# Kernel tuning notes

Hardware: AMD Instinct MI355X
Metric: run time of the kernel (lower is better)

Reference implementation:

```python
import jax, jax.numpy as jnp
import numpy as np
from jax import lax

FC = 8      # heads_count
LN_EPS = 1e-5

def _ln(x, g, b):
    mu = jnp.mean(x, axis=-1, keepdims=True)
    var = jnp.mean((x - mu) ** 2, axis=-1, keepdims=True)
    return (x - mu) / jnp.sqrt(var + LN_EPS) * g + b

def _l2norm(x):
    return x / jnp.maximum(jnp.linalg.norm(x, axis=-1, keepdims=True), 1e-12)

def _gelu(x):
    return jax.nn.gelu(x, approximate=False)

def _resize_bilinear(x, oh, ow):
    # x: [N, C, H, W], align_corners=True bilinear (matches F.interpolate)
    h, w = x.shape[2], x.shape[3]
    ys = jnp.linspace(0.0, h - 1.0, oh)
    xs = jnp.linspace(0.0, w - 1.0, ow)
    y0 = jnp.floor(ys).astype(jnp.int32); y1 = jnp.minimum(y0 + 1, h - 1)
    x0 = jnp.floor(xs).astype(jnp.int32); x1 = jnp.minimum(x0 + 1, w - 1)
    dy = (ys - y0).astype(x.dtype)[None, None, :, None]
    dx = (xs - x0).astype(x.dtype)[None, None, None, :]
    rows = x[:, :, y0, :] * (1 - dy) + x[:, :, y1, :] * dy
    return rows[:, :, :, x0] * (1 - dx) + rows[:, :, :, x1] * dx

def _merge_block(x, center, h, w, p):
    # x: [n,l,c], center: [n,s,c]
    n, l, c = x.shape
    hc, wc = h // 2, w // 2
    xn = x.transpose(0, 2, 1).reshape(n, c, h, w)
    cn = center.transpose(0, 2, 1).reshape(n, c, hc, wc)
    up = _resize_bilinear(cn, h, w)
    y = jnp.concatenate([xn, up], axis=1)            # [n,2c,h,w]
    y = y.transpose(0, 2, 3, 1)                      # NHWC
    y = _gelu(y @ p['mb_l0_w'] + p['mb_l0_b'])
    y = y @ p['mb_l1_w'] + p['mb_l1_b']              # [n,h,w,c]
    y = y.transpose(0, 3, 1, 2)                      # NCHW
    mu = jnp.mean(y, axis=(1, 2, 3), keepdims=True)  # GroupNorm(1, c)
    var = jnp.mean((y - mu) ** 2, axis=(1, 2, 3), keepdims=True)
    y = (y - mu) / jnp.sqrt(var + LN_EPS) * p['mb_gn_g'][None, :, None, None] + p['mb_gn_b'][None, :, None, None]
    down = _resize_bilinear(y, hc, wc)
    new_x = y.reshape(n, c, h * w).transpose(0, 2, 1) + x
    new_c = down.reshape(n, c, hc * wc).transpose(0, 2, 1) + center
    return new_x, new_c

def _global_cluster(x0, center1, p):
    n, l, c = x0.shape
    s = center1.shape[1]
    xp = x0 @ p['gc_p0_w'] + p['gc_p0_b']            # [n,l,hd]
    cp = center1 @ p['gc_p1_w'] + p['gc_p1_b']       # [n,s,2hd]
    hd = xp.shape[-1]
    sc = hd // FC
    m = n * FC
    xp = xp.reshape(n, l, FC, sc).transpose(0, 2, 1, 3).reshape(m, l, sc)
    cp = cp.reshape(n, s, FC, 2 * sc).transpose(0, 2, 1, 3).reshape(m, s, 2 * sc)
    cpt, cval = cp[..., :sc], cp[..., sc:]
    sim = jnp.einsum('mlc,msc->mls', _l2norm(xp), _l2norm(cpt))
    sim = jax.nn.sigmoid(p['gc_alpha'] * sim + p['gc_beta'])
    vals = jnp.max(sim, axis=2)                      # [m,l]
    idx = jnp.argmax(sim, axis=2)                    # [m,l]
    disp = vals[..., None] * jnp.take_along_axis(cval, idx[:, :, None], axis=1)  # [m,l,sc]
    disp = disp.reshape(n, FC, l, sc).transpose(0, 2, 1, 3).reshape(n, l, FC * sc)
    return disp @ p['gc_m_w'] + p['gc_m_b']

def _global_block(x0, center1, h, w, p):
    n, l, c = x0.shape
    new = _global_cluster(x0, center1, p)
    new = _ln(new, p['gb_n0_g'], p['gb_n0_b'])
    y = jnp.concatenate([x0, new], axis=2)           # [n,l,2c]
    y = y.reshape(n, h, w, 2 * c)
    y = _gelu(y @ p['gb_lin_w'] + p['gb_lin_b'])     # [n,h,w,2c]
    y = y.transpose(0, 3, 1, 2)                      # NCHW
    y = lax.conv_general_dilated(y, p['gb_conv_w'], (1, 1), ((1, 1), (1, 1)),
                                 dimension_numbers=('NCHW', 'OIHW', 'NCHW'))
    y = y + p['gb_conv_b'][None, :, None, None]
    y = y.reshape(n, c, h * w).transpose(0, 2, 1)    # [n,l,c]
    return _ln(y, p['gb_n1_g'], p['gb_n1_b']) + x0

def setup_inputs() -> dict:
    key = jax.random.key(0)
    ks = jax.random.split(key, 24)
    N, H, W, C, HD = 8, 52, 52, 256, 256
    L = H * W
    S = (H // 2) * (W // 2)
    f32 = jnp.float32
    def xav(k, shape, fin, fout):
        a = (6.0 / (fin + fout)) ** 0.5
        return jax.random.uniform(k, shape, minval=-a, maxval=a, dtype=f32)
    return {
        'x0_16x': jax.random.normal(ks[0], (N, L, C), f32),
        'x1_16x': jax.random.normal(ks[1], (N, L, C), f32),
        'x0_32x': jax.random.normal(ks[2], (N, S, C), f32),
        'x1_32x': jax.random.normal(ks[3], (N, S, C), f32),
        'size0_16x': 52, 'size1_16x': 52,
        'mb_l0_w': xav(ks[4], (2 * C, 2 * C), 2 * C, 2 * C), 'mb_l0_b': jnp.zeros((2 * C,), f32),
        'mb_l1_w': xav(ks[5], (2 * C, C), 2 * C, C), 'mb_l1_b': jnp.zeros((C,), f32),
        'mb_gn_g': jnp.ones((C,), f32), 'mb_gn_b': jnp.zeros((C,), f32),
        'gc_p0_w': xav(ks[6], (C, HD), C, HD), 'gc_p0_b': jnp.zeros((HD,), f32),
        'gc_p1_w': xav(ks[7], (C, 2 * HD), C, 2 * HD), 'gc_p1_b': jnp.zeros((2 * HD,), f32),
        'gc_m_w': xav(ks[8], (HD, C), HD, C), 'gc_m_b': jnp.zeros((C,), f32),
        'gc_alpha': jnp.ones((1,), f32), 'gc_beta': jnp.zeros((1,), f32),
        'gb_n0_g': jnp.ones((C,), f32), 'gb_n0_b': jnp.zeros((C,), f32),
        'gb_lin_w': xav(ks[9], (2 * C, 2 * C), 2 * C, 2 * C), 'gb_lin_b': jnp.zeros((2 * C,), f32),
        'gb_conv_w': xav(ks[10], (C, 2 * C, 3, 3), 2 * C * 9, C * 9), 'gb_conv_b': jnp.zeros((C,), f32),
        'gb_n1_g': jnp.ones((C,), f32), 'gb_n1_b': jnp.zeros((C,), f32),
    }

def reference(x0_16x, x1_16x, x0_32x, x1_32x, size0_16x, size1_16x,
              mb_l0_w, mb_l0_b, mb_l1_w, mb_l1_b, mb_gn_g, mb_gn_b,
              gc_p0_w, gc_p0_b, gc_p1_w, gc_p1_b, gc_m_w, gc_m_b, gc_alpha, gc_beta,
              gb_n0_g, gb_n0_b, gb_lin_w, gb_lin_b, gb_conv_w, gb_conv_b, gb_n1_g, gb_n1_b):
    p = dict(mb_l0_w=mb_l0_w, mb_l0_b=mb_l0_b, mb_l1_w=mb_l1_w, mb_l1_b=mb_l1_b,
             mb_gn_g=mb_gn_g, mb_gn_b=mb_gn_b,
             gc_p0_w=gc_p0_w, gc_p0_b=gc_p0_b, gc_p1_w=gc_p1_w, gc_p1_b=gc_p1_b,
             gc_m_w=gc_m_w, gc_m_b=gc_m_b, gc_alpha=gc_alpha, gc_beta=gc_beta,
             gb_n0_g=gb_n0_g, gb_n0_b=gb_n0_b, gb_lin_w=gb_lin_w, gb_lin_b=gb_lin_b,
             gb_conv_w=gb_conv_w, gb_conv_b=gb_conv_b, gb_n1_g=gb_n1_g, gb_n1_b=gb_n1_b)
    h0 = w0 = int(size0_16x)
    h1 = w1 = int(size1_16x)
    # single layer, type == 'cross' (types=["cross"]); shared weights across streams
    x0_16x, x0_32x = _merge_block(x0_16x, x0_32x, h0, w0, p)
    x1_16x, x1_32x = _merge_block(x1_16x, x1_32x, h1, w1, p)
    x0_16x = _global_block(x0_16x, x1_32x, h0, w0, p)
    x1_16x = _global_block(x1_16x, x0_32x, h1, w1, p)
    return (x0_16x, x1_16x)
```

## Files before the change

### kernel.cpp

```cpp
#include <hip/hip_runtime.h>
#include <math.h>

#define NB 8
#define HH 52
#define WW 52
#define LL 2704
#define CC 256
#define HC 26
#define WC 26
#define SS 676
#define C2 512
#define FCn 8
#define SCn 32
#define M16 (NB*LL)
#define M32 (NB*SS)
#define KCONV (9*C2)
#define SAMP16 ((size_t)LL*CC)
#define SAMP32 ((size_t)SS*CC)

typedef double dvec4 __attribute__((ext_vector_type(4)));
typedef float  f32x4 __attribute__((ext_vector_type(4)));
typedef short  b16x8 __attribute__((ext_vector_type(8)));

__device__ __forceinline__ float  gelu_ct(float x){ return 0.5f*x*(1.0f + erff(x*0.70710678118654752f)); }
__device__ __forceinline__ double gelu_ct(double x){ return 0.5*x*(1.0 + erf(x*0.70710678118654752440)); }

__device__ __forceinline__ short f2b(float x){
    union { float f; unsigned u; } v; v.f = x;
    unsigned r = v.u + 0x7fffu + ((v.u >> 16) & 1u);
    return (short)(r >> 16);
}

template<typename TA0, typename TA1, typename TO, bool GELU, bool CAT>
__global__ __launch_bounds__(256) void gemm_d64(
    const TA0* __restrict__ A0, const TA1* __restrict__ A1, int K0,
    const float* __restrict__ W, const float* __restrict__ Bias,
    TO* __restrict__ Out, int M, int K, int N)
{
    __shared__ double As[32][65];
    __shared__ double Bs[32][65];
    const int t = threadIdx.x;
    const int mBase = blockIdx.y * 64;
    const int nBase = blockIdx.x * 64;
    const int arow = t >> 2;
    const int kofA = (t & 3) << 3;
    const int kb   = (t >> 4) << 1;
    const int nof  = (t & 15) << 2;
    const int w  = t >> 6;
    const int wr = (w >> 1) * 32;
    const int wc = (w & 1) * 32;
    const int lane = t & 63;
    const int lr = lane & 15, lk = lane >> 4;

    dvec4 prm = {0.,0.,0.,0.}, prn = {0.,0.,0.,0.};
    prm = __builtin_amdgcn_mfma_f64_16x16x4f64((double)lr, 0.25, prm, 0,0,0);
    prn = __builtin_amdgcn_mfma_f64_16x16x4f64(0.25, (double)lr, prn, 0,0,0);
    int pm[4], pn[4];
    #pragma unroll
    for (int i=0;i<4;i++){ pm[i] = (int)prm[i]; pn[i] = (int)prn[i]; }

    dvec4 acc00 = {0.,0.,0.,0.}, acc01 = {0.,0.,0.,0.};
    dvec4 acc10 = {0.,0.,0.,0.}, acc11 = {0.,0.,0.,0.};
    const int am = mBase + arow;

    double aReg[8], bReg[8];
    auto loadA = [&](int k0){
        #pragma unroll
        for (int j=0;j<8;j++){
            int k = k0 + kofA + j;
            double v = 0.0;
            if (am < M){
                if (!CAT || k < K0) v = (double)A0[(size_t)am*K0 + k];
                else                v = (double)A1[(size_t)am*(K-K0) + (k-K0)];
            }
            aReg[j] = v;
        }
    };
    auto loadB = [&](int k0){
        #pragma unroll
        for (int r=0;r<2;r++)
            #pragma unroll
            for (int j=0;j<4;j++)
                bReg[r*4+j] = (double)W[(size_t)(k0+kb+r)*N + nBase + nof + j];
    };
    loadA(0); loadB(0);
    for (int k0 = 0; k0 < K; k0 += 32){
        __syncthreads();
        #pragma unroll
        for (int j=0;j<8;j++) As[kofA+j][arow] = aReg[j];
        #pragma unroll
        for (int r=0;r<2;r++)
            #pragma unroll
            for (int j=0;j<4;j++) Bs[kb+r][nof+j] = bReg[r*4+j];
        __syncthreads();
        if (k0 + 32 < K){ loadA(k0+32); loadB(k0+32); }
        #pragma unroll
        for (int ks = 0; ks < 8; ks++){
            double a0 = As[ks*4+lk][wr+lr];
            double a1 = As[ks*4+lk][wr+16+lr];
            double b0 = Bs[ks*4+lk][wc+lr];
            double b1 = Bs[ks*4+lk][wc+16+lr];
            acc00 = __builtin_amdgcn_mfma_f64_16x16x4f64(a0,b0,acc00,0,0,0);
            acc01 = __builtin_amdgcn_mfma_f64_16x16x4f64(a0,b1,acc01,0,0,0);
            acc10 = __builtin_amdgcn_mfma_f64_16x16x4f64(a1,b0,acc10,0,0,0);
            acc11 = __builtin_amdgcn_mfma_f64_16x16x4f64(a1,b1,acc11,0,0,0);
        }
    }
    #pragma unroll
    for (int i=0;i<4;i++){
        const int gm0 = mBase + wr + pm[i];
        const int gm1 = gm0 + 16;
        const int gn0 = nBase + wc + pn[i];
        const int gn1 = gn0 + 16;
        const double bias0 = (double)Bias[gn0];
        const double bias1 = (double)Bias[gn1];
        if (gm0 < M){
            double v0 = acc00[i] + bias0; if (GELU) v0 = gelu_ct(v0);
            double v1 = acc01[i] + bias1; if (GELU) v1 = gelu_ct(v1);
            Out[(size_t)gm0*N + gn0] = (TO)v0;
            Out[(size_t)gm0*N + gn1] = (TO)v1;
        }
        if (gm1 < M){
            double v0 = acc10[i] + bias0; if (GELU) v0 = gelu_ct(v0);
            double v1 = acc11[i] + bias1; if (GELU) v1 = gelu_ct(v1);
            Out[(size_t)gm1*N + gn0] = (TO)v0;
            Out[(size_t)gm1*N + gn1] = (TO)v1;
        }
    }
}

template<bool GELU, bool CAT, bool OUT_BF>
__global__ __launch_bounds__(256) void gemm_bf(
    const short* __restrict__ A0, const short* __restrict__ A1, int K0,
    const short* __restrict__ Wb, const float* __restrict__ Bias,
    void* __restrict__ OutV, int M, int K, int N)
{
    __shared__ short As[64][72];
    __shared__ short Bs[64][72];
    const int t = threadIdx.x;
    const int mBase = blockIdx.y*64, nBase = blockIdx.x*64;
    const int lane = t & 63, lr = lane & 15, lg = lane >> 4;
    const int wr = (t >> 6) * 16;
    const int srow = t >> 2;
    const int sk   = (t & 3) * 16;
    const int am = mBase + srow;
    const int bo = nBase + srow;
    f32x4 acc[4] = {{0,0,0,0},{0,0,0,0},{0,0,0,0},{0,0,0,0}};

    for (int c0 = 0; c0 < K; c0 += 64){
        const int kk = c0 + sk;
        const short* ap;
        if (!CAT || kk < K0) ap = A0 + (size_t)am*K0 + kk;
        else                 ap = A1 + (size_t)am*(K-K0) + (kk - K0);
        b16x8 a0 = *(const b16x8*)ap;
        b16x8 a1 = *(const b16x8*)(ap + 8);
        b16x8 bv0 = *(const b16x8*)&Wb[(size_t)bo*K + kk];
        b16x8 bv1 = *(const b16x8*)&Wb[(size_t)bo*K + kk + 8];
        __syncthreads();
        *(b16x8*)&As[srow][sk]     = a0;
        *(b16x8*)&As[srow][sk + 8] = a1;
        *(b16x8*)&Bs[srow][sk]     = bv0;
        *(b16x8*)&Bs[srow][sk + 8] = bv1;
        __syncthreads();
        #pragma unroll
        for (int kc=0;kc<2;kc++){
            b16x8 a = *(const b16x8*)&As[wr + lr][kc*32 + lg*8];
            #pragma unroll
            for (int cb=0;cb<4;cb++){
                b16x8 b = *(const b16x8*)&Bs[cb*16 + lr][kc*32 + lg*8];
                acc[cb] = __builtin_amdgcn_mfma_f32_16x16x32_bf16(a, b, acc[cb], 0,0,0);
            }
        }
    }
    #pragma unroll
    for (int cb=0;cb<4;cb++){
        int col = nBase + cb*16 + lr;
        float bias = Bias[col];
        #pragma unroll
        for (int i=0;i<4;i++){
            int row = mBase + wr + lg*4 + i;
            float v = acc[cb][i] + bias;
            if (GELU) v = gelu_ct(v);
            if (OUT_BF) ((short*)OutV)[(size_t)row*N + col] = f2b(v);
            else        ((float*)OutV)[(size_t)row*N + col] = v;
        }
    }
}

__global__ __launch_bounds__(256) void conv_bf2(const short* __restrict__ Xb,
    const short* __restrict__ WTb, const float* __restrict__ Bias, float* __restrict__ Out)
{
    __shared__ short As[32][72];
    __shared__ short Bs[256][72];
    const int t = threadIdx.x;
    const int mBase = blockIdx.x*32;
    const int lane = t & 63, lr = lane & 15, lg = lane >> 4;
    const int w = t >> 6;
    const int wr16 = (w & 1) * 16;
    const int ch   = (w >> 1) * 8;
    const int arow = t >> 3;
    const int ska  = (t & 7) * 8;
    const int srow = t >> 2;
    const int sk   = (t & 3) * 16;
    const int am = mBase + arow;
    const int an = am / LL; const int ahw = am % LL;
    const int ah = ahw / WW; const int aw = ahw % WW;
    f32x4 acc[8];
    #pragma unroll
    for (int i=0;i<8;i++) acc[i] = (f32x4){0.f,0.f,0.f,0.f};
    const b16x8 z = {0,0,0,0,0,0,0,0};

    for (int pos = 0; pos < 9; pos++){
        const int dh = pos/3 - 1, dw = pos%3 - 1;
        const int h2 = ah + dh, w2 = aw + dw;
        const bool ok = (h2 >= 0 && h2 < HH && w2 >= 0 && w2 < WW);
        const short* xrow = Xb + ((size_t)(an*LL + h2*WW + w2))*C2;
        for (int c0 = 0; c0 < C2; c0 += 64){
            b16x8 a0 = ok ? *(const b16x8*)&xrow[c0 + ska] : z;
            b16x8 w0[4], w1[4];
            #pragma unroll
            for (int r=0;r<4;r++){
                const short* wp = WTb + (size_t)(srow + 64*r)*KCONV + pos*C2 + c0 + sk;
                w0[r] = *(const b16x8*)wp;
                w1[r] = *(const b16x8*)(wp + 8);
            }
            __syncthreads();
            *(b16x8*)&As[arow][ska] = a0;
            #pragma unroll
            for (int r=0;r<4;r++){
                *(b16x8*)&Bs[srow + 64*r][sk]     = w0[r];
                *(b16x8*)&Bs[srow + 64*r][sk + 8] = w1[r];
            }
            __syncthreads();
            #pragma unroll
            for (int kc=0;kc<2;kc++){
                b16x8 a = *(const b16x8*)&As[wr16 + lr][kc*32 + lg*8];
                #pragma unroll
                for (int cb=0;cb<8;cb++){
                    b16x8 b = *(const b16x8*)&Bs[(ch+cb)*16 + lr][kc*32 + lg*8];
                    acc[cb] = __builtin_amdgcn_mfma_f32_16x16x32_bf16(a, b, acc[cb], 0,0,0);
                }
            }
        }
    }
    #pragma unroll
    for (int cb=0;cb<8;cb++){
        int col = (ch+cb)*16 + lr;
        float bias = Bias[col];
        #pragma unroll
        for (int i=0;i<4;i++){
            int row = mBase + wr16 + lg*4 + i;
            Out[(size_t)row*CC + col] = acc[cb][i] + bias;
        }
    }
}

__global__ void wtransb_k(const float* __restrict__ wsrc, short* __restrict__ wt){
    int o = blockIdx.x;
    int i = threadIdx.x;
    #pragma unroll
    for (int pos = 0; pos < 9; pos++)
        wt[(size_t)o*KCONV + pos*C2 + i] = f2b(wsrc[((size_t)o*C2 + i)*9 + pos]);
}

__global__ void wtb_k(const float* __restrict__ src, short* __restrict__ dst, int K, int N){
    int n = blockIdx.x;
    for (int k = threadIdx.x; k < K; k += 256)
        dst[(size_t)n*K + k] = f2b(src[(size_t)k*N + n]);
}

__global__ void d2b_k(const double* __restrict__ src, short* __restrict__ dst){
    int i = blockIdx.x*256 + threadIdx.x;
    dst[i] = f2b((float)src[i]);
}

__global__ void ups_k(const float* __restrict__ cen, double* __restrict__ up){
    int idx = blockIdx.x*256 + threadIdx.x;
    int c = idx & 255;
    int gl = idx >> 8;
    int n = gl / LL, l = gl % LL;
    int h = l / WW, w = l % WW;
    double fy = (h==HH-1) ? (double)(HC-1) : h*((double)(HC-1)/(HH-1));
    double fx = (w==WW-1) ? (double)(WC-1) : w*((double)(WC-1)/(WW-1));
    int y0 = (int)fy; int y1 = min(y0+1, HC-1);
    int x0 = (int)fx; int x1 = min(x0+1, WC-1);
    double dy = fy - y0, dx = fx - x0;
    const float* base = cen + (size_t)n*SAMP32 + c;
    double v00 = (double)base[(size_t)(y0*WC + x0)*CC];
    double v01 = (double)base[(size_t)(y0*WC + x1)*CC];
    double v10 = (double)base[(size_t)(y1*WC + x0)*CC];
    double v11 = (double)base[(size_t)(y1*WC + x1)*CC];
    double r0 = v00*(1.0-dy) + v10*dy;
    double r1 = v01*(1.0-dy) + v11*dy;
    up[idx] = r0*(1.0-dx) + r1*dx;
}

__global__ __launch_bounds__(256) void gn_stats_k(const double* __restrict__ t2c,
    double* __restrict__ stats, int nOff){
    const double* p = t2c + (size_t)blockIdx.y*SAMP16;
    int i0 = blockIdx.x*4096 + threadIdx.x;
    double s = 0.0, q = 0.0;
    #pragma unroll
    for (int r = 0; r < 16; r++){
        double v = p[i0 + r*256];
        s += v; q += v*v;
    }
    #pragma unroll
    for (int off = 32; off; off >>= 1){
        s += __shfl_xor(s, off);
        q += __shfl_xor(q, off);
    }
    __shared__ double ls[4], lq[4];
    int wid = threadIdx.x >> 6;
    if ((threadIdx.x & 63) == 0){ ls[wid] = s; lq[wid] = q; }
    __syncthreads();
    if (threadIdx.x == 0){
        int n = nOff + blockIdx.y;
        atomicAdd(&stats[n*2+0], ls[0]+ls[1]+ls[2]+ls[3]);
        atomicAdd(&stats[n*2+1], lq[0]+lq[1]+lq[2]+lq[3]);
    }
}

__global__ void merge_x_k(const double* __restrict__ t2c, const float* __restrict__ x,
    const float* __restrict__ g, const float* __restrict__ b,
    const double* __restrict__ stats, int nOff, double* __restrict__ mxn){
    int idx = blockIdx.x*256 + threadIdx.x;
    const double inv = 1.0/((double)LL*CC);
    int c = idx & (CC-1);
    int n = nOff + idx / (LL*CC);
    double mu = stats[2*n]*inv;
    double var = stats[2*n+1]*inv - mu*mu;
    double r = 1.0/sqrt(var + 1e-5);
    mxn[idx] = (t2c[idx]-mu)*r*(double)g[c] + (double)b[c] + (double)x[idx];
}

__global__ void merge_c_k(const double* __restrict__ t2c, const float* __restrict__ cen,
    const float* __restrict__ g, const float* __restrict__ b,
    const double* __restrict__ stats, int nOff, double* __restrict__ mcn){
    int idx = blockIdx.x*256 + threadIdx.x;
    int c = idx & 255;
    int ns = idx >> 8;
    int nl = ns / SS, s = ns % SS;
    int i = s / WC, j = s % WC;
    double fy = (i==WC-1) ? (double)(HH-1) : i*((double)(HH-1)/(HC-1));
    double fx = (j==WC-1) ? (double)(WW-1) : j*((double)(WW-1)/(WC-1));
    int y0 = (int)fy; int y1 = min(y0+1, HH-1);
    int x0 = (int)fx; int x1 = min(x0+1, WW-1);
    double dy = fy - y0, dx = fx - x0;
    const double* base = t2c + (size_t)nl*SAMP16 + c;
    double v00 = base[(size_t)(y0*WW + x0)*CC];
    double v01 = base[(size_t)(y0*WW + x1)*CC];
    double v10 = base[(size_t)(y1*WW + x0)*CC];
    double v11 = base[(size_t)(y1*WW + x1)*CC];
    double r0 = v00*(1.0-dy) + v10*dy;
    double r1 = v01*(1.0-dy) + v11*dy;
    double v = r0*(1.0-dx) + r1*dx;
    const double inv = 1.0/((double)LL*CC);
    int n = nOff + nl;
    double mu = stats[2*n]*inv;
    double var = stats[2*n+1]*inv - mu*mu;
    double r = 1.0/sqrt(var + 1e-5);
    mcn[idx] = (v-mu)*r*(double)g[c] + (double)b[c] + (double)cen[idx];
}

__global__ __launch_bounds__(256) void cptn_k(const double* __restrict__ cp, double* __restrict__ ctn){
    int ns = blockIdx.x;
    int n = ns / SS, s = ns % SS;
    int hgrp = threadIdx.x >> 5, k = threadIdx.x & 31;
    double v = cp[(size_t)ns*C2 + hgrp*64 + k];
    double q = v*v;
    #pragma unroll
    for (int off = 16; off; off >>= 1) q += __shfl_xor(q, off, 32);
    double d = fmax(sqrt(q), 1e-12);
    ctn[((size_t)(n*FCn + hgrp)*SS + s)*SCn + k] = v/d;
}

__global__ __launch_bounds__(256) void norm_k(const double* __restrict__ xpc, double* __restrict__ norms){
    int t = threadIdx.x;
    int g = t >> 5, k = t & 31;
    int gl = blockIdx.x*8 + g;
    int nl = gl / LL, l = gl % LL;
    int h = blockIdx.y;
    double v = xpc[(size_t)gl*CC + h*SCn + k];
    double q = v*v;
    #pragma unroll
    for (int off = 16; off; off >>= 1) q += __shfl_xor(q, off, 32);
    if (k == 0) norms[((size_t)nl*FCn + h)*LL + l] = fmax(sqrt(q), 1e-12);
}

__global__ __launch_bounds__(256) void sim3_k(
    const double* __restrict__ xpc,
    const double* __restrict__ norms,
    const double* __restrict__ ctn,
    const double* __restrict__ cp,
    const float* __restrict__ alpha_p, const float* __restrict__ beta_p,
    int nOff, short* __restrict__ dispb)
{
    __shared__ double xs[32][65];
    __shared__ double cs[32][65];
    const int t = threadIdx.x;
    const int lBase = blockIdx.x * 64;
    const int h = blockIdx.y;
    const int nl = blockIdx.z;
    const int n = nOff + nl;
    const int w  = t >> 6;
    const int wr = (w >> 1) * 32;
    const int wc = (w & 1) * 32;
    const int lane = t & 63;
    const int lr = lane & 15, lk = lane >> 4;
    const double alpha = (double)alpha_p[0], beta = (double)beta_p[0];
    const double sgn = (alpha >= 0.0) ? 1.0 : -1.0;

    dvec4 prm = {0.,0.,0.,0.}, prn = {0.,0.,0.,0.};
    prm = __builtin_amdgcn_mfma_f64_16x16x4f64((double)lr, 0.25, prm, 0,0,0);
    prn = __builtin_amdgcn_mfma_f64_16x16x4f64(0.25, (double)lr, prn, 0,0,0);
    int pm[4], pn[4];
    #pragma unroll
    for (int i=0;i<4;i++){ pm[i] = (int)prm[i]; pn[i] = (int)prn[i]; }

    const int lav = min(64, LL - lBase);
    #pragma unroll
    for (int r = 0; r < 8; r++){
        int idx = t + r*256;
        int li = idx >> 5, ki = idx & 31;
        double v = 0.0;
        if (li < lav) v = xpc[((size_t)nl*LL + lBase + li)*CC + h*SCn + ki];
        xs[ki][li] = v;
    }

    double bz[2][2][4];
    int    bs[2][2][4];
    #pragma unroll
    for (int rf=0; rf<2; rf++)
        #pragma unroll
        for (int j=0; j<2; j++)
            #pragma unroll
            for (int i=0; i<4; i++){ bz[rf][j][i] = -1.0e300; bs[rf][j][i] = 0; }

    const double* cbase = ctn + ((size_t)(n*FCn + h))*SS*SCn;
    for (int sBase = 0; sBase < SS; sBase += 64){
        const int sav = min(64, SS - sBase);
        const double* cb = cbase + (size_t)sBase*SCn;
        __syncthreads();
        #pragma unroll
        for (int r = 0; r < 8; r++){
            int idx = t + r*256;
            int si = idx >> 5, ki = idx & 31;
            cs[ki][si] = (si < sav) ? cb[idx] : 0.0;
        }
        __syncthreads();
        dvec4 a00 = {0.,0.,0.,0.}, a01 = {0.,0.,0.,0.};
        dvec4 a10 = {0.,0.,0.,0.}, a11 = {0.,0.,0.,0.};
        #pragma unroll
        for (int ks = 0; ks < 8; ks++){
            double xa0 = xs[ks*4+lk][wr+lr];
            double xa1 = xs[ks*4+lk][wr+16+lr];
            double cb0 = cs[ks*4+lk][wc+lr];
            double cb1 = cs[ks*4+lk][wc+16+lr];
            a00 = __builtin_amdgcn_mfma_f64_16x16x4f64(xa0,cb0,a00,0,0,0);
            a01 = __builtin_amdgcn_mfma_f64_16x16x4f64(xa0,cb1,a01,0,0,0);
            a10 = __builtin_amdgcn_mfma_f64_16x16x4f64(xa1,cb0,a10,0,0,0);
            a11 = __builtin_amdgcn_mfma_f64_16x16x4f64(xa1,cb1,a11,0,0,0);
        }
        #pragma unroll
        for (int i=0;i<4;i++){
            int s0 = sBase + wc + pn[i];
            int s1 = s0 + 16;
            if (s0 < SS){
                double z = sgn*a00[i];
                if (z > bz[0][0][i]){ bz[0][0][i] = z; bs[0][0][i] = s0; }
                z = sgn*a10[i];
                if (z > bz[1][0][i]){ bz[1][0][i] = z; bs[1][0][i] = s0; }
            }
            if (s1 < SS){
                double z = sgn*a01[i];
                if (z > bz[0][1][i]){ bz[0][1][i] = z; bs[0][1][i] = s1; }
                z = sgn*a11[i];
                if (z > bz[1][1][i]){ bz[1][1][i] = z; bs[1][1][i] = s1; }
            }
        }
    }
    __syncthreads();
    double* redv = &xs[0][0];
    int*    redi = (int*)&cs[0][0];
    #pragma unroll
    for (int rf=0; rf<2; rf++){
        #pragma unroll
        for (int i=0;i<4;i++){
            double z0 = bz[rf][0][i]; int i0 = bs[rf][0][i];
            double z1 = bz[rf][1][i]; int i1 = bs[rf][1][i];
            bool take1 = (z1 > z0) || (z1 == z0 && i1 < i0);
            double z = take1 ? z1 : z0;
            int    s = take1 ? i1 : i0;
            int row = wr + rf*16 + pm[i];
            int cls = (w & 1)*16 + pn[i];
            redv[row*32 + cls] = z;
            redi[row*32 + cls] = s;
        }
    }
    __syncthreads();
    if (t < 64){
        double best = redv[t*32]; int bi = redi[t*32];
        #pragma unroll
        for (int c = 1; c < 32; c++){
            double v = redv[t*32 + c]; int ii = redi[t*32 + c];
            if (v > best || (v == best && ii < bi)){ best = v; bi = ii; }
        }
        int l = lBase + t;
        if (l < LL){
            double nrm = norms[((size_t)nl*FCn + h)*LL + l];
            double zb = alpha*((sgn*best)/nrm) + beta;
            double val;
            if (zb >= 0.0) val = 1.0/(1.0 + exp(-zb));
            else { double e = exp(zb); val = e/(1.0+e); }
            const double* cv = cp + ((size_t)(n*SS + bi))*C2 + h*64 + 32;
            short* dr = dispb + ((size_t)(n*LL + l))*CC + h*SCn;
            #pragma unroll
            for (int k=0;k<32;k++) dr[k] = f2b((float)(val*cv[k]));
        }
    }
}

__global__ __launch_bounds__(256) void ln_bf_k(const float* __restrict__ y,
    const float* __restrict__ g, const float* __restrict__ b, short* __restrict__ ob){
    int row = blockIdx.x*4 + (threadIdx.x >> 6);
    int lane = threadIdx.x & 63;
    const float* rp = y + (size_t)row*CC;
    float4 v = *(const float4*)(rp + lane*4);
    float s = v.x+v.y+v.z+v.w;
    float q = v.x*v.x+v.y*v.y+v.z*v.z+v.w*v.w;
    #pragma unroll
    for (int off = 32; off; off >>= 1){ s += __shfl_xor(s, off); q += __shfl_xor(q, off); }
    float mu = s*(1.0f/CC);
    float var = q*(1.0f/CC) - mu*mu;
    float r = rsqrtf(var + 1e-5f);
    int c = lane*4;
    float4 gv = *(const float4*)(g+c);
    float4 bv = *(const float4*)(b+c);
    short* op = ob + (size_t)row*CC + c;
    op[0] = f2b((v.x-mu)*r*gv.x+bv.x);
    op[1] = f2b((v.y-mu)*r*gv.y+bv.y);
    op[2] = f2b((v.z-mu)*r*gv.z+bv.z);
    op[3] = f2b((v.w-mu)*r*gv.w+bv.w);
}

__global__ __launch_bounds__(256) void final_k(float* __restrict__ y, const double* __restrict__ res,
    const float* __restrict__ g, const float* __restrict__ b){
    int row = blockIdx.x*4 + (threadIdx.x >> 6);
    int lane = threadIdx.x & 63;
    float* rp = y + (size_t)row*CC;
    const double* xp = res + (size_t)row*CC;
    float4 v = *(const float4*)(rp + lane*4);
    float s = v.x+v.y+v.z+v.w;
    float q = v.x*v.x+v.y*v.y+v.z*v.z+v.w*v.w;
    #pragma unroll
    for (int off = 32; off; off >>= 1){ s += __shfl_xor(s, off); q += __shfl_xor(q, off); }
    float mu = s*(1.0f/CC);
    float var = q*(1.0f/CC) - mu*mu;
    float r = rsqrtf(var + 1e-5f);
    int c = lane*4;
    float4 gv = *(const float4*)(g+c);
    float4 bv = *(const float4*)(b+c);
    float4 o;
    o.x = (v.x-mu)*r*gv.x+bv.x + (float)xp[c+0];
    o.y = (v.y-mu)*r*gv.y+bv.y + (float)xp[c+1];
    o.z = (v.z-mu)*r*gv.z+bv.z + (float)xp[c+2];
    o.w = (v.w-mu)*r*gv.w+bv.w + (float)xp[c+3];
    *(float4*)(rp+c) = o;
}

extern "C" void kernel_launch(void* const* d_in, const int* in_sizes, int n_in,
                              void* d_out, int out_size, void* d_ws, size_t ws_size,
                              hipStream_t stream)
{
    const float* x16[2] = {(const float*)d_in[0], (const float*)d_in[1]};
    const float* x32[2] = {(const float*)d_in[2], (const float*)d_in[3]};
    const float* mb_l0_w = (const float*)d_in[6];
    const float* mb_l0_b = (const float*)d_in[7];
    const float* mb_l1_w = (const float*)d_in[8];
    const float* mb_l1_b = (const float*)d_in[9];
    const float* mb_gn_g = (const float*)d_in[10];
    const float* mb_gn_b = (const float*)d_in[11];
    const float* gc_p0_w = (const float*)d_in[12];
    const float* gc_p0_b = (const float*)d_in[13];
    const float* gc_p1_w = (const float*)d_in[14];
    const float* gc_p1_b = (const float*)d_in[15];
    const float* gc_m_w  = (const float*)d_in[16];
    const float* gc_m_b  = (const float*)d_in[17];
    const float* gc_alpha= (const float*)d_in[18];
    const float* gc_beta = (const float*)d_in[19];
    const float* gb_n0_g = (const float*)d_in[20];
    const float* gb_n0_b = (const float*)d_in[21];
    const float* gb_lin_w= (const float*)d_in[22];
    const float* gb_lin_b= (const float*)d_in[23];
    const float* gb_conv_w=(const float*)d_in[24];
    const float* gb_conv_b=(const float*)d_in[25];
    const float* gb_n1_g = (const float*)d_in[26];
    const float* gb_n1_b = (const float*)d_in[27];

    const size_t F8  = (size_t)M16*CC*8;
    const size_t G8  = (size_t)M32*CC*8;
    const size_t WT4 = (size_t)KCONV*CC*4;

    char* base = (char*)d_ws;
    double* mx[2] = { (double*)base, (double*)(base + F8) };
    double* mc[2] = { (double*)(base + 2*F8), (double*)(base + 2*F8 + G8) };
    char*   pWT   = base + 2*F8 + 2*G8;
    short*  WTb   = (short*)pWT;
    short*  WLb   = (short*)(pWT + 2359296);
    short*  WMb   = (short*)(pWT + 2883584);
    double* stats = (double*)(pWT + WT4);
    char*   E     = pWT + WT4 + 256;
    const size_t base_need = 2*F8 + 2*G8 + WT4 + 256;

    const size_t T2  = (size_t)LL*CC*8;
    const size_t T1  = (size_t)LL*C2*8;
    const size_t TN  = (size_t)FCn*LL*8;
    int nb = 1;
    {
        const int cands[4] = {8,4,2,1};
        for (int ci = 0; ci < 4; ci++){
            int c = cands[ci];
            size_t merge_r  = (size_t)c*(2*T2 + T1);
            size_t global_r = 22151168ull + 11075584ull + (size_t)c*(T2 + TN) + 11075584ull + 11075584ull;
            size_t r = merge_r > global_r ? merge_r : global_r;
            if (base_need + r <= ws_size){ nb = c; break; }
            if (c == 1) return;
        }
    }

    double* t2c = (double*)E;
    double* t1c = (double*)(E + nb*T2);
    double* upc = (double*)(E + nb*(T2 + T1));
    double* cp    = (double*)E;
    double* ctn   = (double*)(E + 22151168);
    double* xpc   = (double*)(E + 33226752);
    double* norms = (double*)(E + 33226752 + nb*T2);
    short*  dispb = (short*) (E + 33226752 + (size_t)nb*(T2 + TN));
    short*  mxb   = (short*) (E + 33226752 + (size_t)nb*(T2 + TN) + 11075584);
    float*  Dbuf  = (float*) E;
    short*  Dbufb = (short*) (E + 22151168);
    short*  Bbufb = (short*) E;

    wtransb_k<<<CC, C2, 0, stream>>>(gb_conv_w, WTb);
    wtb_k<<<C2, 256, 0, stream>>>(gb_lin_w, WLb, C2, C2);
    wtb_k<<<CC, 256, 0, stream>>>(gc_m_w, WMb, CC, CC);

    const int Mc = nb*LL;
    const int mTiles = (Mc + 63) / 64;

    for (int i = 0; i < 2; i++){
        hipMemsetAsync(stats, 0, 16*sizeof(double), stream);
        for (int ch = 0; ch < NB; ch += nb){
            const float* x16c = x16[i] + (size_t)ch*SAMP16;
            const float* x32c = x32[i] + (size_t)ch*SAMP32;
            ups_k<<<nb*LL, 256, 0, stream>>>(x32c, upc);
            gemm_d64<float,double,double,true,true><<<dim3(8, mTiles), 256, 0, stream>>>(
                x16c, upc, CC, mb_l0_w, mb_l0_b, t1c, Mc, C2, C2);
            gemm_d64<double,double,double,false,false><<<dim3(4, mTiles), 256, 0, stream>>>(
                t1c, (const double*)nullptr, C2, mb_l1_w, mb_l1_b, t2c, Mc, C2, CC);
            gn_stats_k<<<dim3(169, nb), 256, 0, stream>>>(t2c, stats, ch);
            merge_x_k<<<nb*LL, 256, 0, stream>>>(t2c, x16c,
                mb_gn_g, mb_gn_b, stats, ch, mx[i] + (size_t)ch*SAMP16);
            merge_c_k<<<nb*SS, 256, 0, stream>>>(t2c, x32c,
                mb_gn_g, mb_gn_b, stats, ch, mc[i] + (size_t)ch*SAMP32);
        }
    }

    float* outp[2] = { (float*)d_out, (float*)d_out + (size_t)M16*CC };
    for (int i = 0; i < 2; i++){
        const double* xi64 = mx[i];
        const double* ci64 = mc[1-i];
        gemm_d64<double,double,double,false,false><<<dim3(8, 85), 256, 0, stream>>>(
            ci64, (const double*)nullptr, CC, gc_p1_w, gc_p1_b, cp, M32, CC, C2);
        cptn_k<<<M32, 256, 0, stream>>>(cp, ctn);
        for (int ch = 0; ch < NB; ch += nb){
            gemm_d64<double,double,double,false,false><<<dim3(4, mTiles), 256, 0, stream>>>(
                xi64 + (size_t)ch*SAMP16, (const double*)nullptr, CC, gc_p0_w, gc_p0_b,
                xpc, Mc, CC, CC);
            norm_k<<<dim3(nb*(LL/8), FCn), 256, 0, stream>>>(xpc, norms);
            sim3_k<<<dim3((LL+63)/64, FCn, nb), 256, 0, stream>>>(
                xpc, norms, ctn, cp, gc_alpha, gc_beta, ch, dispb);
        }
        d2b_k<<<(M16*CC)/256, 256, 0, stream>>>(xi64, mxb);
        gemm_bf<false,false,false><<<dim3(4, 338), 256, 0, stream>>>(
            dispb, (const short*)nullptr, CC, WMb, gc_m_b, Dbuf, M16, CC, CC);
        ln_bf_k<<<M16/4, 256, 0, stream>>>(Dbuf, gb_n0_g, gb_n0_b, Dbufb);
        gemm_bf<true,true,true><<<dim3(8, 338), 256, 0, stream>>>(
            mxb, Dbufb, CC, WLb, gb_lin_b, Bbufb, M16, C2, C2);
        conv_bf2<<<M16/32, 256, 0, stream>>>(Bbufb, WTb, gb_conv_b, outp[i]);
        final_k<<<M16/4, 256, 0, stream>>>(outp[i], xi64, gb_n1_g, gb_n1_b);
    }
}
```

Measured before the change: 2.383 ms.

## Project centers before upsampling and enlarge FP64 GEMM tile to 128x64

Bilinear upsampling is linear, so the upsampled half of the first merge-block linear layer is now computed at coarse resolution (a GEMM over the 26x26 centers with the lower half of the weights). The result is upsampled inside the epilogue of the fine-resolution GEMM, which now only has K=256. This removes the ups_k kernel and halves the K of the large GEMM. The FP64 MFMA GEMM tile also grows from 64x64 to 128x64 with 8 accumulators per wave, giving more reuse per LDS load. The cost is epilogue gather traffic and higher register pressure.

```diff
diff --git a/kernel.cpp b/kernel.cpp
--- a/kernel.cpp
+++ b/kernel.cpp
@@ -31,24 +31,23 @@
     return (short)(r >> 16);
 }
 
-template<typename TA0, typename TA1, typename TO, bool GELU, bool CAT>
+template<typename TA0, typename TO, bool GELU, bool ADDB, bool UPS>
 __global__ __launch_bounds__(256) void gemm_d64(
-    const TA0* __restrict__ A0, const TA1* __restrict__ A1, int K0,
+    const TA0* __restrict__ A0,
     const float* __restrict__ W, const float* __restrict__ Bias,
+    const double* __restrict__ cw,
     TO* __restrict__ Out, int M, int K, int N)
 {
-    __shared__ double As[32][65];
-    __shared__ double Bs[32][65];
+    __shared__ double As[32][130];
+    __shared__ double Bs[32][66];
     const int t = threadIdx.x;
-    const int mBase = blockIdx.y * 64;
+    const int mBase = blockIdx.y * 128;
     const int nBase = blockIdx.x * 64;
-    const int arow = t >> 2;
-    const int kofA = (t & 3) << 3;
+    const int arow = t >> 1;
+    const int kofA = (t & 1) << 4;
     const int kb   = (t >> 4) << 1;
     const int nof  = (t & 15) << 2;
     const int w  = t >> 6;
-    const int wr = (w >> 1) * 32;
-    const int wc = (w & 1) * 32;
     const int lane = t & 63;
     const int lr = lane & 15, lk = lane >> 4;
 
@@ -59,21 +58,19 @@
     #pragma unroll
     for (int i=0;i<4;i++){ pm[i] = (int)prm[i]; pn[i] = (int)prn[i]; }
 
-    dvec4 acc00 = {0.,0.,0.,0.}, acc01 = {0.,0.,0.,0.};
-    dvec4 acc10 = {0.,0.,0.,0.}, acc11 = {0.,0.,0.,0.};
+    dvec4 acc[2][4];
+    #pragma unroll
+    for (int rf=0;rf<2;rf++)
+        #pragma unroll
+        for (int cb=0;cb<4;cb++) acc[rf][cb] = (dvec4){0.,0.,0.,0.};
+
     const int am = mBase + arow;
-
-    double aReg[8], bReg[8];
+    double aReg[16], bReg[8];
     auto loadA = [&](int k0){
         #pragma unroll
-        for (int j=0;j<8;j++){
+        for (int j=0;j<16;j++){
             int k = k0 + kofA + j;
-            double v = 0.0;
-            if (am < M){
-                if (!CAT || k < K0) v = (double)A0[(size_t)am*K0 + k];
-                else                v = (double)A1[(size_t)am*(K-K0) + (k-K0)];
-            }
-            aReg[j] = v;
+            aReg[j] = (am < M) ? (double)A0[(size_t)am*K + k] : 0.0;
         }
     };
     auto loadB = [&](int k0){
@@ -87,7 +84,7 @@
     for (int k0 = 0; k0 < K; k0 += 32){
         __syncthreads();
         #pragma unroll
-        for (int j=0;j<8;j++) As[kofA+j][arow] = aReg[j];
+        for (int j=0;j<16;j++) As[kofA+j][arow] = aReg[j];
         #pragma unroll
         for (int r=0;r<2;r++)
             #pragma unroll
@@ -96,35 +93,58 @@
         if (k0 + 32 < K){ loadA(k0+32); loadB(k0+32); }
         #pragma unroll
         for (int ks = 0; ks < 8; ks++){
-            double a0 = As[ks*4+lk][wr+lr];
-            double a1 = As[ks*4+lk][wr+16+lr];
-            double b0 = Bs[ks*4+lk][wc+lr];
-            double b1 = Bs[ks*4+lk][wc+16+lr];
-            acc00 = __builtin_amdgcn_mfma_f64_16x16x4f64(a0,b0,acc00,0,0,0);
-            acc01 = __builtin_amdgcn_mfma_f64_16x16x4f64(a0,b1,acc01,0,0,0);
-            acc10 = __builtin_amdgcn_mfma_f64_16x16x4f64(a1,b0,acc10,0,0,0);
-            acc11 = __builtin_amdgcn_mfma_f64_16x16x4f64(a1,b1,acc11,0,0,0);
-        }
-    }
-    #pragma unroll
-    for (int i=0;i<4;i++){
-        const int gm0 = mBase + wr + pm[i];
-        const int gm1 = gm0 + 16;
-        const int gn0 = nBase + wc + pn[i];
-        const int gn1 = gn0 + 16;
-        const double bias0 = (double)Bias[gn0];
-        const double bias1 = (double)Bias[gn1];
-        if (gm0 < M){
-            double v0 = acc00[i] + bias0; if (GELU) v0 = gelu_ct(v0);
-            double v1 = acc01[i] + bias1; if (GELU) v1 = gelu_ct(v1);
-            Out[(size_t)gm0*N + gn0] = (TO)v0;
-            Out[(size_t)gm0*N + gn1] = (TO)v1;
-        }
-        if (gm1 < M){
-            double v0 = acc10[i] + bias0; if (GELU) v0 = gelu_ct(v0);
-            double v1 = acc11[i] + bias1; if (GELU) v1 = gelu_ct(v1);
-            Out[(size_t)gm1*N + gn0] = (TO)v0;
-            Out[(size_t)gm1*N + gn1] = (TO)v1;
+            double a0 = As[ks*4+lk][w*32 + lr];
+            double a1 = As[ks*4+lk][w*32 + 16 + lr];
+            double b0 = Bs[ks*4+lk][lr];
+            double b1 = Bs[ks*4+lk][16 + lr];
+            double b2 = Bs[ks*4+lk][32 + lr];
+            double b3 = Bs[ks*4+lk][48 + lr];
+            acc[0][0] = __builtin_amdgcn_mfma_f64_16x16x4f64(a0,b0,acc[0][0],0,0,0);
+            acc[0][1] = __builtin_amdgcn_mfma_f64_16x16x4f64(a0,b1,acc[0][1],0,0,0);
+            acc[0][2] = __builtin_amdgcn_mfma_f64_16x16x4f64(a0,b2,acc[0][2],0,0,0);
+            acc[0][3] = __builtin_amdgcn_mfma_f64_16x16x4f64(a0,b3,acc[0][3],0,0,0);
+            acc[1][0] = __builtin_amdgcn_mfma_f64_16x16x4f64(a1,b0,acc[1][0],0,0,0);
+            acc[1][1] = __builtin_amdgcn_mfma_f64_16x16x4f64(a1,b1,acc[1][1],0,0,0);
+            acc[1][2] = __builtin_amdgcn_mfma_f64_16x16x4f64(a1,b2,acc[1][2],0,0,0);
+            acc[1][3] = __builtin_amdgcn_mfma_f64_16x16x4f64(a1,b3,acc[1][3],0,0,0);
+        }
+    }
+    #pragma unroll
+    for (int rf=0;rf<2;rf++){
+        #pragma unroll
+        for (int i=0;i<4;i++){
+            const int row = mBase + w*32 + rf*16 + pm[i];
+            if (row >= M) continue;
+            int nloc = 0, y0=0, y1=0, x0=0, x1=0;
+            double dy=0.0, dx=0.0;
+            if (UPS){
+                nloc = row / LL;
+                int l = row - nloc*LL;
+                int hh = l / WW, ww2 = l - hh*WW;
+                double fy = (hh==HH-1) ? (double)(HC-1) : hh*((double)(HC-1)/(HH-1));
+                double fx = (ww2==WW-1) ? (double)(WC-1) : ww2*((double)(WC-1)/(WW-1));
+                y0 = (int)fy; y1 = min(y0+1, HC-1);
+                x0 = (int)fx; x1 = min(x0+1, WC-1);
+                dy = fy - y0; dx = fx - x0;
+            }
+            #pragma unroll
+            for (int cb=0;cb<4;cb++){
+                const int col = nBase + cb*16 + pn[i];
+                double v = acc[rf][cb][i];
+                if (UPS){
+                    const double* cb0 = cw + ((size_t)nloc*SS)*N + col;
+                    double v00 = cb0[(size_t)(y0*WC + x0)*N];
+                    double v01 = cb0[(size_t)(y0*WC + x1)*N];
+                    double v10 = cb0[(size_t)(y1*WC + x0)*N];
+                    double v11 = cb0[(size_t)(y1*WC + x1)*N];
+                    double r0 = v00*(1.0-dy) + v10*dy;
+                    double r1 = v01*(1.0-dy) + v11*dy;
+                    v += r0*(1.0-dx) + r1*dx;
+                }
+                if (ADDB) v += (double)Bias[col];
+                if (GELU) v = gelu_ct(v);
+                Out[(size_t)row*N + col] = (TO)v;
+            }
         }
     }
 }
@@ -272,27 +292,6 @@
 __global__ void d2b_k(const double* __restrict__ src, short* __restrict__ dst){
     int i = blockIdx.x*256 + threadIdx.x;
     dst[i] = f2b((float)src[i]);
-}
-
-__global__ void ups_k(const float* __restrict__ cen, double* __restrict__ up){
-    int idx = blockIdx.x*256 + threadIdx.x;
-    int c = idx & 255;
-    int gl = idx >> 8;
-    int n = gl / LL, l = gl % LL;
-    int h = l / WW, w = l % WW;
-    double fy = (h==HH-1) ? (double)(HC-1) : h*((double)(HC-1)/(HH-1));
-    double fx = (w==WW-1) ? (double)(WC-1) : w*((double)(WC-1)/(WW-1));
-    int y0 = (int)fy; int y1 = min(y0+1, HC-1);
-    int x0 = (int)fx; int x1 = min(x0+1, WC-1);
-    double dy = fy - y0, dx = fx - x0;
-    const float* base = cen + (size_t)n*SAMP32 + c;
-    double v00 = (double)base[(size_t)(y0*WC + x0)*CC];
-    double v01 = (double)base[(size_t)(y0*WC + x1)*CC];
-    double v10 = (double)base[(size_t)(y1*WC + x0)*CC];
-    double v11 = (double)base[(size_t)(y1*WC + x1)*CC];
-    double r0 = v00*(1.0-dy) + v10*dy;
-    double r1 = v01*(1.0-dy) + v11*dy;
-    up[idx] = r0*(1.0-dx) + r1*dx;
 }
 
 __global__ __launch_bounds__(256) void gn_stats_k(const double* __restrict__ t2c,
@@ -615,13 +614,14 @@
 
     const size_t T2  = (size_t)LL*CC*8;
     const size_t T1  = (size_t)LL*C2*8;
+    const size_t TC  = (size_t)SS*C2*8;
     const size_t TN  = (size_t)FCn*LL*8;
     int nb = 1;
     {
         const int cands[4] = {8,4,2,1};
         for (int ci = 0; ci < 4; ci++){
             int c = cands[ci];
-            size_t merge_r  = (size_t)c*(2*T2 + T1);
+            size_t merge_r  = (size_t)c*(T2 + T1 + TC);
             size_t global_r = 22151168ull + 11075584ull + (size_t)c*(T2 + TN) + 11075584ull + 11075584ull;
             size_t r = merge_r > global_r ? merge_r : global_r;
             if (base_need + r <= ws_size){ nb = c; break; }
@@ -631,7 +631,7 @@
 
     double* t2c = (double*)E;
     double* t1c = (double*)(E + nb*T2);
-    double* upc = (double*)(E + nb*(T2 + T1));
+    double* cwb = (double*)(E + nb*(T2 + T1));
     double* cp    = (double*)E;
     double* ctn   = (double*)(E + 22151168);
     double* xpc   = (double*)(E + 33226752);
@@ -647,18 +647,21 @@
     wtb_k<<<CC, 256, 0, stream>>>(gc_m_w, WMb, CC, CC);
 
     const int Mc = nb*LL;
-    const int mTiles = (Mc + 63) / 64;
+    const int Ms = nb*SS;
+    const int mTiles  = (Mc + 127) / 128;
+    const int sTiles  = (Ms + 127) / 128;
 
     for (int i = 0; i < 2; i++){
         hipMemsetAsync(stats, 0, 16*sizeof(double), stream);
         for (int ch = 0; ch < NB; ch += nb){
             const float* x16c = x16[i] + (size_t)ch*SAMP16;
             const float* x32c = x32[i] + (size_t)ch*SAMP32;
-            ups_k<<<nb*LL, 256, 0, stream>>>(x32c, upc);
-            gemm_d64<float,double,double,true,true><<<dim3(8, mTiles), 256, 0, stream>>>(
-                x16c, upc, CC, mb_l0_w, mb_l0_b, t1c, Mc, C2, C2);
-            gemm_d64<double,double,double,false,false><<<dim3(4, mTiles), 256, 0, stream>>>(
-                t1c, (const double*)nullptr, C2, mb_l1_w, mb_l1_b, t2c, Mc, C2, CC);
+            gemm_d64<float,double,false,false,false><<<dim3(8, sTiles), 256, 0, stream>>>(
+                x32c, mb_l0_w + (size_t)CC*C2, mb_l0_b, nullptr, cwb, Ms, CC, C2);
+            gemm_d64<float,double,true,true,true><<<dim3(8, mTiles), 256, 0, stream>>>(
+                x16c, mb_l0_w, mb_l0_b, cwb, t1c, Mc, CC, C2);
+            gemm_d64<double,double,false,true,false><<<dim3(4, mTiles), 256, 0, stream>>>(
+                t1c, mb_l1_w, mb_l1_b, nullptr, t2c, Mc, C2, CC);
             gn_stats_k<<<dim3(169, nb), 256, 0, stream>>>(t2c, stats, ch);
             merge_x_k<<<nb*LL, 256, 0, stream>>>(t2c, x16c,
                 mb_gn_g, mb_gn_b, stats, ch, mx[i] + (size_t)ch*SAMP16);
@@ -671,13 +674,12 @@
     for (int i = 0; i < 2; i++){
         const double* xi64 = mx[i];
         const double* ci64 = mc[1-i];
-        gemm_d64<double,double,double,false,false><<<dim3(8, 85), 256, 0, stream>>>(
-            ci64, (const double*)nullptr, CC, gc_p1_w, gc_p1_b, cp, M32, CC, C2);
+        gemm_d64<double,double,false,true,false><<<dim3(8, (M32+127)/128), 256, 0, stream>>>(
+            ci64, gc_p1_w, gc_p1_b, nullptr, cp, M32, CC, C2);
         cptn_k<<<M32, 256, 0, stream>>>(cp, ctn);
         for (int ch = 0; ch < NB; ch += nb){
-            gemm_d64<double,double,double,false,false><<<dim3(4, mTiles), 256, 0, stream>>>(
-                xi64 + (size_t)ch*SAMP16, (const double*)nullptr, CC, gc_p0_w, gc_p0_b,
-                xpc, Mc, CC, CC);
+            gemm_d64<double,double,false,true,false><<<dim3(4, mTiles), 256, 0, stream>>>(
+                xi64 + (size_t)ch*SAMP16, gc_p0_w, gc_p0_b, nullptr, xpc, Mc, CC, CC);
             norm_k<<<dim3(nb*(LL/8), FCn), 256, 0, stream>>>(xpc, norms);
             sim3_k<<<dim3((LL+63)/64, FCn, nb), 256, 0, stream>>>(
                 xpc, norms, ctn, cp, gc_alpha, gc_beta, ch, dispb);
```

Result: slower. 2.453 ms (+3.0%).
